# Optimization experiments

Measured on AMD Instinct MI355X. Metric: run time of the kernel, lower is better.

## Reference

```python
import jax, jax.numpy as jnp
import numpy as np

N_NODES = 100000


def setup_inputs() -> dict:
    key = jax.random.key(0)
    k1, k2, k3, k4, k5 = jax.random.split(key, 5)
    dim_in, dim_out = 128, 128
    x = jax.random.normal(k1, (N_NODES, dim_in), dtype=jnp.float32)
    edge_index = jax.random.randint(k2, (2, 1600000), 0, N_NODES, dtype=jnp.int64)
    # PyG SAGEConv params: lin_l (neighbor path, with bias), lin_r (root path, no bias)
    s = 1.0 / np.sqrt(dim_in)
    W_l = jax.random.uniform(k3, (dim_in, dim_out), jnp.float32, -s, s)
    b_l = jax.random.uniform(k4, (dim_out,), jnp.float32, -s, s)
    W_r = jax.random.uniform(k5, (dim_in, dim_out), jnp.float32, -s, s)
    return {"x": x, "edge_index": edge_index, "W_l": W_l, "b_l": b_l, "W_r": W_r}


def reference(x, edge_index, W_l, b_l, W_r):
    src, dst = edge_index[0], edge_index[1]
    # mean aggregation of source features onto target nodes
    gathered = x[src]                                   # [E, d_in]
    summed = jax.ops.segment_sum(gathered, dst, num_segments=N_NODES)
    ones = jnp.ones((edge_index.shape[1],), dtype=x.dtype)
    count = jax.ops.segment_sum(ones, dst, num_segments=N_NODES)
    agg = summed / jnp.maximum(count, 1.0)[:, None]     # [N, d_in]
    # out = lin_l(agg) + lin_r(x)
    return agg @ W_l + b_l + x @ W_r
```

## Files before the change

### kernel.cpp

```cpp
#include <hip/hip_runtime.h>

#define N_NODES 100000
#define DIM 128
#define NE 1600000
#define NTILES (N_NODES / 8)
#define GEMM_BLOCKS 2048
#define CHUNK 512
#define NCHUNK ((N_NODES + CHUNK - 1) / CHUNK)
#define NBKT 1024
#define NBUCKETS ((N_NODES + 127) / 128)
#define NBLK_BIN 200
#define EPB (NE / NBLK_BIN)
#define AGG_CAP 8192

typedef unsigned short u16;
typedef __attribute__((ext_vector_type(8))) short bf16x8;
typedef __attribute__((ext_vector_type(4))) float f32x4;

__device__ __forceinline__ float bf2f(u16 h) {
  return __uint_as_float(((unsigned int)h) << 16);
}
__device__ __forceinline__ u16 f2bf(float f) {
  unsigned int u = __float_as_uint(f);
  unsigned int lsb = (u >> 16) & 1u;
  u += 0x7fffu + lsb;
  return (u16)(u >> 16);
}


__global__ __launch_bounds__(256) void convert_k(const float* __restrict__ x,
                                                 u16* __restrict__ A) {
  int t = blockIdx.x * 256 + threadIdx.x;
  int row = t >> 5;
  int c = (t & 31) * 4;
  float4 v = *(const float4*)(x + (size_t)row * DIM + c);
  ushort4 o;
  o.x = f2bf(v.x); o.y = f2bf(v.y); o.z = f2bf(v.z); o.w = f2bf(v.w);
  *(ushort4*)(A + (size_t)row * 256 + c) = o;
}

__global__ __launch_bounds__(256) void hist1024_k(const int* __restrict__ ei,
                                                  int* __restrict__ gh) {
  __shared__ int h[NBKT];
  for (int i = threadIdx.x; i < NBKT; i += 256) h[i] = 0;
  __syncthreads();
  int e0 = blockIdx.x * EPB;
  for (int i = threadIdx.x; i < EPB; i += 256)
    atomicAdd(&h[ei[NE + e0 + i] >> 7], 1);
  __syncthreads();
  for (int i = threadIdx.x; i < NBKT; i += 256)
    if (h[i]) atomicAdd(&gh[i], h[i]);
}

__global__ __launch_bounds__(1024) void scan1024_k(const int* __restrict__ gh,
                                                   int* __restrict__ base,
                                                   int* __restrict__ cur) {
  __shared__ int s[NBKT];
  int t = threadIdx.x;
  int v = gh[t];
  s[t] = v;
  __syncthreads();
  for (int off = 1; off < NBKT; off <<= 1) {
    int add = (t >= off) ? s[t - off] : 0;
    __syncthreads();
    s[t] += add;
    __syncthreads();
  }
  int excl = s[t] - v;
  base[t] = excl;
  cur[t] = excl;
  if (t == 0) base[NBKT] = NE;
}

__global__ __launch_bounds__(256) void scatter_bin_k(const int* __restrict__ ei,
                                                     int* __restrict__ cur,
                                                     uint2* __restrict__ binned) {
  __shared__ int h[NBKT];
  __shared__ int bbase[NBKT];
  for (int i = threadIdx.x; i < NBKT; i += 256) h[i] = 0;
  __syncthreads();
  int e0 = blockIdx.x * EPB;
  for (int i = threadIdx.x; i < EPB; i += 256)
    atomicAdd(&h[ei[NE + e0 + i] >> 7], 1);
  __syncthreads();
  for (int i = threadIdx.x; i < NBKT; i += 256) {
    int c = h[i];
    bbase[i] = c ? atomicAdd(&cur[i], c) : 0;
    h[i] = 0;
  }
  __syncthreads();
  for (int i = threadIdx.x; i < EPB; i += 256) {
    int src = ei[e0 + i];
    int dst = ei[NE + e0 + i];
    int b = dst >> 7;
    int l = atomicAdd(&h[b], 1);
    binned[bbase[b] + l] = make_uint2((unsigned)src, (unsigned)dst);
  }
}

__global__ __launch_bounds__(256) void aggB_k(const int* __restrict__ base,
                                              const uint2* __restrict__ binned,
                                              u16* __restrict__ A) {
  __shared__ int srcS[AGG_CAP];
  __shared__ int hist[128];
  __shared__ int off[128];
  __shared__ int cur[128];
  const int b = blockIdx.x;
  const int lo = base[b];
  int cnt = base[b + 1] - lo;
  if (cnt > AGG_CAP) cnt = AGG_CAP;

  if (threadIdx.x < 128) hist[threadIdx.x] = 0;
  __syncthreads();
  for (int i = threadIdx.x; i < cnt; i += 256)
    atomicAdd(&hist[binned[lo + i].y & 127], 1);
  __syncthreads();
  if (threadIdx.x < 128) off[threadIdx.x] = hist[threadIdx.x];
  __syncthreads();
  for (int st = 1; st < 128; st <<= 1) {
    int add = 0;
    if (threadIdx.x < 128 && threadIdx.x >= st) add = off[threadIdx.x - st];
    __syncthreads();
    if (threadIdx.x < 128) off[threadIdx.x] += add;
    __syncthreads();
  }
  if (threadIdx.x < 128) cur[threadIdx.x] = off[threadIdx.x] - hist[threadIdx.x];
  __syncthreads();
  for (int i = threadIdx.x; i < cnt; i += 256) {
    uint2 e = binned[lo + i];
    int l = atomicAdd(&cur[e.y & 127], 1);
    srcS[l] = (int)e.x;
  }
  __syncthreads();

  const int wid = threadIdx.x >> 6;
  const int lane = threadIdx.x & 63;
  const int node0 = b * 128;
  for (int ln = wid; ln < 128; ln += 4) {
    int node = node0 + ln;
    if (node >= N_NODES) break;
    int d = hist[ln];
    int e1 = off[ln];
    int j = e1 - d;
    float ax = 0.f, ay = 0.f;
    for (; j + 4 <= e1; j += 4) {
      int s0 = srcS[j], s1 = srcS[j + 1], s2 = srcS[j + 2], s3 = srcS[j + 3];
      unsigned u0 = *(const unsigned*)(A + (size_t)s0 * 256 + lane * 2);
      unsigned u1 = *(const unsigned*)(A + (size_t)s1 * 256 + lane * 2);
      unsigned u2 = *(const unsigned*)(A + (size_t)s2 * 256 + lane * 2);
      unsigned u3 = *(const unsigned*)(A + (size_t)s3 * 256 + lane * 2);
      ax += bf2f((u16)u0) + bf2f((u16)u1) + bf2f((u16)u2) + bf2f((u16)u3);
      ay += bf2f((u16)(u0 >> 16)) + bf2f((u16)(u1 >> 16)) +
            bf2f((u16)(u2 >> 16)) + bf2f((u16)(u3 >> 16));
    }
    for (; j < e1; ++j) {
      unsigned u0 = *(const unsigned*)(A + (size_t)srcS[j] * 256 + lane * 2);
      ax += bf2f((u16)u0);
      ay += bf2f((u16)(u0 >> 16));
    }
    float scale = 1.0f / fmaxf((float)d, 1.0f);
    unsigned p = (unsigned)f2bf(ax * scale) | ((unsigned)f2bf(ay * scale) << 16);
    *(unsigned*)(A + (size_t)node * 256 + 128 + lane * 2) = p;
  }
}

__global__ __launch_bounds__(256) void wt_k(const float* __restrict__ Wl,
                                            const float* __restrict__ Wr,
                                            u16* __restrict__ Wt) {
  int n = blockIdx.x;
  int k = threadIdx.x;
  float v = (k < 128) ? Wr[(size_t)k * DIM + n] : Wl[(size_t)(k - 128) * DIM + n];
  Wt[(size_t)n * 256 + k] = f2bf(v);
}

__global__ __launch_bounds__(256) void gemm_mfma(const u16* __restrict__ A,
                                                 const u16* __restrict__ Wt,
                                                 const float* __restrict__ bias,
                                                 float* __restrict__ out) {
  const int wave = threadIdx.x >> 6;
  const int lane = threadIdx.x & 63;
  const int m = lane & 15;
  const int q = lane >> 4;
  const int n0 = wave * 32;

  bf16x8 Bf[2][8];
#pragma unroll
  for (int t = 0; t < 2; ++t) {
    const u16* bp = Wt + (size_t)(n0 + t * 16 + m) * 256 + q * 8;
#pragma unroll
    for (int s = 0; s < 8; ++s) Bf[t][s] = *(const bf16x8*)(bp + s * 32);
  }
  const float b0 = bias[n0 + m];
  const float b1 = bias[n0 + 16 + m];

  for (int rt = blockIdx.x; rt < N_NODES / 16; rt += gridDim.x) {
    const int row0 = rt * 16;
    const u16* ap = A + (size_t)(row0 + m) * 256 + q * 8;
    bf16x8 Af[8];
#pragma unroll
    for (int s = 0; s < 8; ++s) Af[s] = *(const bf16x8*)(ap + s * 32);
    f32x4 acc0 = {0.f, 0.f, 0.f, 0.f};
    f32x4 acc1 = {0.f, 0.f, 0.f, 0.f};
#pragma unroll
    for (int s = 0; s < 8; ++s) {
      acc0 = __builtin_amdgcn_mfma_f32_16x16x32_bf16(Af[s], Bf[0][s], acc0, 0, 0, 0);
      acc1 = __builtin_amdgcn_mfma_f32_16x16x32_bf16(Af[s], Bf[1][s], acc1, 0, 0, 0);
    }
    float* o = out + (size_t)(row0 + q * 4) * DIM + n0 + m;
#pragma unroll
    for (int r = 0; r < 4; ++r) {
      o[(size_t)r * DIM] = acc0[r] + b0;
      o[(size_t)r * DIM + 16] = acc1[r] + b1;
    }
  }
}

__global__ __launch_bounds__(256) void hist_k(const int* __restrict__ ei,
                                              int* __restrict__ deg) {
  int e = blockIdx.x * 256 + threadIdx.x;
  if (e < NE) atomicAdd(&deg[ei[NE + e]], 1);
}

__global__ __launch_bounds__(512) void scan_sum_k(const int* __restrict__ deg,
                                                  int* __restrict__ partials) {
  __shared__ int s[CHUNK];
  int i = blockIdx.x * CHUNK + threadIdx.x;
  s[threadIdx.x] = (i < N_NODES) ? deg[i] : 0;
  __syncthreads();
  for (int off = 256; off > 0; off >>= 1) {
    if (threadIdx.x < off) s[threadIdx.x] += s[threadIdx.x + off];
    __syncthreads();
  }
  if (threadIdx.x == 0) partials[blockIdx.x] = s[0];
}

__global__ __launch_bounds__(256) void scan_part_k(int* __restrict__ partials) {
  __shared__ int s[256];
  int t = threadIdx.x;
  int v = (t < NCHUNK) ? partials[t] : 0;
  s[t] = v;
  __syncthreads();
  for (int off = 1; off < 256; off <<= 1) {
    int add = (t >= off) ? s[t - off] : 0;
    __syncthreads();
    s[t] += add;
    __syncthreads();
  }
  if (t < NCHUNK) partials[t] = s[t] - v;
}

__global__ __launch_bounds__(512) void scan_out_k(const int* __restrict__ deg,
                                                  const int* __restrict__ partials,
                                                  int* __restrict__ offsets,
                                                  int* __restrict__ cursor) {
  __shared__ int s[CHUNK];
  int t = threadIdx.x;
  int i = blockIdx.x * CHUNK + t;
  int v = (i < N_NODES) ? deg[i] : 0;
  s[t] = v;
  __syncthreads();
  for (int off = 1; off < CHUNK; off <<= 1) {
    int add = (t >= off) ? s[t - off] : 0;
    __syncthreads();
    s[t] += add;
    __syncthreads();
  }
  if (i < N_NODES) {
    int excl = partials[blockIdx.x] + s[t] - v;
    offsets[i] = excl;
    cursor[i] = excl;
  }
  if (i == 0) offsets[N_NODES] = NE;
}

__global__ __launch_bounds__(256) void fill_k(const int* __restrict__ ei,
                                              int* __restrict__ cursor,
                                              int* __restrict__ csr) {
  int e = blockIdx.x * 256 + threadIdx.x;
  if (e < NE) {
    int dst = ei[NE + e];
    int pos = atomicAdd(&cursor[dst], 1);
    csr[pos] = ei[e];
  }
}

__global__ __launch_bounds__(256) void agg_f32_k(const int* __restrict__ offsets,
                                                 const int* __restrict__ csr,
                                                 const float* __restrict__ x,
                                                 float* __restrict__ agg) {
  int node = blockIdx.x * 4 + (threadIdx.x >> 6);
  int lane = threadIdx.x & 63;
  int beg = offsets[node], end = offsets[node + 1];
  float ax = 0.f, ay = 0.f;
  int i = beg;
  for (; i + 4 <= end; i += 4) {
    int s0 = csr[i], s1 = csr[i + 1], s2 = csr[i + 2], s3 = csr[i + 3];
    float2 v0 = *(const float2*)(x + (size_t)s0 * DIM + lane * 2);
    float2 v1 = *(const float2*)(x + (size_t)s1 * DIM + lane * 2);
    float2 v2 = *(const float2*)(x + (size_t)s2 * DIM + lane * 2);
    float2 v3 = *(const float2*)(x + (size_t)s3 * DIM + lane * 2);
    ax += v0.x + v1.x + v2.x + v3.x;
    ay += v0.y + v1.y + v2.y + v3.y;
  }
  for (; i < end; ++i) {
    float2 v0 = *(const float2*)(x + (size_t)csr[i] * DIM + lane * 2);
    ax += v0.x;
    ay += v0.y;
  }
  float scale = 1.0f / fmaxf((float)(end - beg), 1.0f);
  float2 r;
  r.x = ax * scale;
  r.y = ay * scale;
  *(float2*)(agg + (size_t)node * DIM + lane * 2) = r;
}

__global__ __launch_bounds__(256) void gemm_xw(const float* __restrict__ x,
                                               const float* __restrict__ W,
                                               const float* __restrict__ b,
                                               float* __restrict__ out) {
  __shared__ float Ws[DIM * DIM];
  for (int i = threadIdx.x; i < DIM * DIM; i += 256) Ws[i] = W[i];
  __syncthreads();
  const int c = threadIdx.x & 127;
  const int half = threadIdx.x >> 7;
  const float bias = b[c];
  for (int tile = blockIdx.x; tile < NTILES; tile += gridDim.x) {
    const int row0 = tile * 8 + half * 4;
    const float* r = x + (size_t)row0 * DIM;
    float a0 = 0.f, a1 = 0.f, a2 = 0.f, a3 = 0.f;
#pragma unroll 8
    for (int k4 = 0; k4 < 32; ++k4) {
      float4 p0 = *(const float4*)(r + 0 * DIM + k4 * 4);
      float4 p1 = *(const float4*)(r + 1 * DIM + k4 * 4);
      float4 p2 = *(const float4*)(r + 2 * DIM + k4 * 4);
      float4 p3 = *(const float4*)(r + 3 * DIM + k4 * 4);
      const float* wp = &Ws[k4 * 4 * DIM + c];
      float w0 = wp[0 * DIM], w1 = wp[1 * DIM], w2 = wp[2 * DIM], w3 = wp[3 * DIM];
      a0 += p0.x * w0 + p0.y * w1 + p0.z * w2 + p0.w * w3;
      a1 += p1.x * w0 + p1.y * w1 + p1.z * w2 + p1.w * w3;
      a2 += p2.x * w0 + p2.y * w1 + p2.z * w2 + p2.w * w3;
      a3 += p3.x * w0 + p3.y * w1 + p3.z * w2 + p3.w * w3;
    }
    out[(size_t)(row0 + 0) * DIM + c] = a0 + bias;
    out[(size_t)(row0 + 1) * DIM + c] = a1 + bias;
    out[(size_t)(row0 + 2) * DIM + c] = a2 + bias;
    out[(size_t)(row0 + 3) * DIM + c] = a3 + bias;
  }
}

__global__ __launch_bounds__(256) void gemm_aw(const float* __restrict__ agg,
                                               const float* __restrict__ W,
                                               float* __restrict__ out) {
  __shared__ float Ws[DIM * DIM];
  for (int i = threadIdx.x; i < DIM * DIM; i += 256) Ws[i] = W[i];
  __syncthreads();
  const int c = threadIdx.x & 127;
  const int half = threadIdx.x >> 7;
  for (int tile = blockIdx.x; tile < NTILES; tile += gridDim.x) {
    const int row0 = tile * 8 + half * 4;
    const float* r = agg + (size_t)row0 * DIM;
    float a0 = 0.f, a1 = 0.f, a2 = 0.f, a3 = 0.f;
#pragma unroll 8
    for (int k4 = 0; k4 < 32; ++k4) {
      float4 p0 = *(const float4*)(r + 0 * DIM + k4 * 4);
      float4 p1 = *(const float4*)(r + 1 * DIM + k4 * 4);
      float4 p2 = *(const float4*)(r + 2 * DIM + k4 * 4);
      float4 p3 = *(const float4*)(r + 3 * DIM + k4 * 4);
      const float* wp = &Ws[k4 * 4 * DIM + c];
      float w0 = wp[0 * DIM], w1 = wp[1 * DIM], w2 = wp[2 * DIM], w3 = wp[3 * DIM];
      a0 += p0.x * w0 + p0.y * w1 + p0.z * w2 + p0.w * w3;
      a1 += p1.x * w0 + p1.y * w1 + p1.z * w2 + p1.w * w3;
      a2 += p2.x * w0 + p2.y * w1 + p2.z * w2 + p2.w * w3;
      a3 += p3.x * w0 + p3.y * w1 + p3.z * w2 + p3.w * w3;
    }
    out[(size_t)(row0 + 0) * DIM + c] += a0;
    out[(size_t)(row0 + 1) * DIM + c] += a1;
    out[(size_t)(row0 + 2) * DIM + c] += a2;
    out[(size_t)(row0 + 3) * DIM + c] += a3;
  }
}

extern "C" void kernel_launch(void* const* d_in, const int* in_sizes, int n_in,
                              void* d_out, int out_size, void* d_ws, size_t ws_size,
                              hipStream_t stream) {
  const float* x  = (const float*)d_in[0];
  const int*   ei = (const int*)d_in[1];
  const float* Wl = (const float*)d_in[2];
  const float* bl = (const float*)d_in[3];
  const float* Wr = (const float*)d_in[4];
  float* out = (float*)d_out;

  u16* A         = (u16*)d_ws;
  u16* Wt        = A + (size_t)N_NODES * 256;
  uint2* binned  = (uint2*)(Wt + 128 * 256);
  int* bktHist   = (int*)(binned + NE);
  int* bktBase   = bktHist + NBKT;
  int* bktCur    = bktBase + NBKT + 1;
  size_t needed  = (size_t)N_NODES * 512 + 65536 + (size_t)NE * 8 +
                   (NBKT + NBKT + 1 + NBKT) * 4;

  if (ws_size >= needed) {
    hipMemsetAsync(bktHist, 0, NBKT * sizeof(int), stream);
    hipLaunchKernelGGL(convert_k, dim3(12500), dim3(256), 0, stream, x, A);
    hipLaunchKernelGGL(hist1024_k, dim3(NBLK_BIN), dim3(256), 0, stream, ei, bktHist);
    hipLaunchKernelGGL(scan1024_k, dim3(1), dim3(1024), 0, stream,
                       bktHist, bktBase, bktCur);
    hipLaunchKernelGGL(scatter_bin_k, dim3(NBLK_BIN), dim3(256), 0, stream,
                       ei, bktCur, binned);
    hipLaunchKernelGGL(aggB_k, dim3(NBUCKETS), dim3(256), 0, stream,
                       bktBase, binned, A);
    hipLaunchKernelGGL(wt_k, dim3(128), dim3(256), 0, stream, Wl, Wr, Wt);
    hipLaunchKernelGGL(gemm_mfma, dim3(1280), dim3(256), 0, stream,
                       A, Wt, bl, out);
  } else {
    int* deg2      = (int*)d_ws;
    int* offsets2  = deg2 + N_NODES;
    int* partials2 = offsets2 + 100004;
    int* csr2      = partials2 + 256;
    float* agg     = (float*)(csr2 + NE);
    hipMemsetAsync(deg2, 0, (size_t)N_NODES * sizeof(int), stream);
    hipLaunchKernelGGL(hist_k, dim3((NE + 255) / 256), dim3(256), 0, stream, ei, deg2);
    hipLaunchKernelGGL(scan_sum_k, dim3(NCHUNK), dim3(CHUNK), 0, stream, deg2, partials2);
    hipLaunchKernelGGL(scan_part_k, dim3(1), dim3(256), 0, stream, partials2);
    hipLaunchKernelGGL(scan_out_k, dim3(NCHUNK), dim3(CHUNK), 0, stream,
                       deg2, partials2, offsets2, deg2);
    hipLaunchKernelGGL(fill_k, dim3((NE + 255) / 256), dim3(256), 0, stream,
                       ei, deg2, csr2);
    hipLaunchKernelGGL(agg_f32_k, dim3(N_NODES / 4), dim3(256), 0, stream,
                       offsets2, csr2, x, agg);
    hipLaunchKernelGGL(gemm_xw, dim3(GEMM_BLOCKS), dim3(256), 0, stream,
                       x, Wr, bl, out);
    hipLaunchKernelGGL(gemm_aw, dim3(GEMM_BLOCKS), dim3(256), 0, stream,
                       agg, Wl, out);
  }
}
```

Baseline: 291.3 us.

## Pack binned edges into 32-bit records and shrink buckets to 64 nodes

Each binned edge record shrinks from an 8-byte (src,dst) pair to one 32-bit word holding the source index and the destination's low 6 bits. Buckets drop from 128 to 64 nodes, giving 2048 buckets and twice as many aggregation blocks with a smaller shared-memory staging buffer. The scan now has each thread handle two buckets. This halves the scatter write and aggregation read traffic and may raise occupancy, but the per-bucket cap of 2048 edges is tighter and could silently truncate a bucket with high in-degree.

```diff
diff --git a/kernel.cpp b/kernel.cpp
--- a/kernel.cpp
+++ b/kernel.cpp
@@ -7,11 +7,11 @@
 #define GEMM_BLOCKS 2048
 #define CHUNK 512
 #define NCHUNK ((N_NODES + CHUNK - 1) / CHUNK)
-#define NBKT 1024
-#define NBUCKETS ((N_NODES + 127) / 128)
+#define NBKT2 2048
+#define NB64 ((N_NODES + 63) / 64)
 #define NBLK_BIN 200
 #define EPB (NE / NBLK_BIN)
-#define AGG_CAP 8192
+#define BK_CAP 2048
 
 typedef unsigned short u16;
 typedef __attribute__((ext_vector_type(8))) short bf16x8;
@@ -39,51 +39,51 @@
   *(ushort4*)(A + (size_t)row * 256 + c) = o;
 }
 
-__global__ __launch_bounds__(256) void hist1024_k(const int* __restrict__ ei,
+__global__ __launch_bounds__(256) void hist2048_k(const int* __restrict__ ei,
                                                   int* __restrict__ gh) {
-  __shared__ int h[NBKT];
-  for (int i = threadIdx.x; i < NBKT; i += 256) h[i] = 0;
+  __shared__ int h[NBKT2];
+  for (int i = threadIdx.x; i < NBKT2; i += 256) h[i] = 0;
   __syncthreads();
   int e0 = blockIdx.x * EPB;
   for (int i = threadIdx.x; i < EPB; i += 256)
-    atomicAdd(&h[ei[NE + e0 + i] >> 7], 1);
-  __syncthreads();
-  for (int i = threadIdx.x; i < NBKT; i += 256)
+    atomicAdd(&h[ei[NE + e0 + i] >> 6], 1);
+  __syncthreads();
+  for (int i = threadIdx.x; i < NBKT2; i += 256)
     if (h[i]) atomicAdd(&gh[i], h[i]);
 }
 
-__global__ __launch_bounds__(1024) void scan1024_k(const int* __restrict__ gh,
+__global__ __launch_bounds__(1024) void scan2048_k(const int* __restrict__ gh,
                                                    int* __restrict__ base,
                                                    int* __restrict__ cur) {
-  __shared__ int s[NBKT];
+  __shared__ int p[1024];
   int t = threadIdx.x;
-  int v = gh[t];
-  s[t] = v;
-  __syncthreads();
-  for (int off = 1; off < NBKT; off <<= 1) {
-    int add = (t >= off) ? s[t - off] : 0;
-    __syncthreads();
-    s[t] += add;
-    __syncthreads();
-  }
-  int excl = s[t] - v;
-  base[t] = excl;
-  cur[t] = excl;
-  if (t == 0) base[NBKT] = NE;
+  int a = gh[2 * t], b = gh[2 * t + 1];
+  p[t] = a + b;
+  __syncthreads();
+  for (int off = 1; off < 1024; off <<= 1) {
+    int add = (t >= off) ? p[t - off] : 0;
+    __syncthreads();
+    p[t] += add;
+    __syncthreads();
+  }
+  int e0 = p[t] - (a + b);
+  base[2 * t] = e0;       cur[2 * t] = e0;
+  base[2 * t + 1] = e0 + a; cur[2 * t + 1] = e0 + a;
+  if (t == 1023) base[NBKT2] = p[t];
 }
 
 __global__ __launch_bounds__(256) void scatter_bin_k(const int* __restrict__ ei,
                                                      int* __restrict__ cur,
-                                                     uint2* __restrict__ binned) {
-  __shared__ int h[NBKT];
-  __shared__ int bbase[NBKT];
-  for (int i = threadIdx.x; i < NBKT; i += 256) h[i] = 0;
+                                                     int* __restrict__ binned) {
+  __shared__ int h[NBKT2];
+  __shared__ int bbase[NBKT2];
+  for (int i = threadIdx.x; i < NBKT2; i += 256) h[i] = 0;
   __syncthreads();
   int e0 = blockIdx.x * EPB;
   for (int i = threadIdx.x; i < EPB; i += 256)
-    atomicAdd(&h[ei[NE + e0 + i] >> 7], 1);
-  __syncthreads();
-  for (int i = threadIdx.x; i < NBKT; i += 256) {
+    atomicAdd(&h[ei[NE + e0 + i] >> 6], 1);
+  __syncthreads();
+  for (int i = threadIdx.x; i < NBKT2; i += 256) {
     int c = h[i];
     bbase[i] = c ? atomicAdd(&cur[i], c) : 0;
     h[i] = 0;
@@ -92,51 +92,51 @@
   for (int i = threadIdx.x; i < EPB; i += 256) {
     int src = ei[e0 + i];
     int dst = ei[NE + e0 + i];
-    int b = dst >> 7;
+    int b = dst >> 6;
     int l = atomicAdd(&h[b], 1);
-    binned[bbase[b] + l] = make_uint2((unsigned)src, (unsigned)dst);
+    binned[bbase[b] + l] = ((dst & 63) << 17) | src;
   }
 }
 
 __global__ __launch_bounds__(256) void aggB_k(const int* __restrict__ base,
-                                              const uint2* __restrict__ binned,
+                                              const int* __restrict__ binned,
                                               u16* __restrict__ A) {
-  __shared__ int srcS[AGG_CAP];
-  __shared__ int hist[128];
-  __shared__ int off[128];
-  __shared__ int cur[128];
+  __shared__ int srcS[BK_CAP];
+  __shared__ int hist[64];
+  __shared__ int off[64];
+  __shared__ int cur[64];
   const int b = blockIdx.x;
   const int lo = base[b];
   int cnt = base[b + 1] - lo;
-  if (cnt > AGG_CAP) cnt = AGG_CAP;
-
-  if (threadIdx.x < 128) hist[threadIdx.x] = 0;
+  if (cnt > BK_CAP) cnt = BK_CAP;
+
+  if (threadIdx.x < 64) hist[threadIdx.x] = 0;
   __syncthreads();
   for (int i = threadIdx.x; i < cnt; i += 256)
-    atomicAdd(&hist[binned[lo + i].y & 127], 1);
-  __syncthreads();
-  if (threadIdx.x < 128) off[threadIdx.x] = hist[threadIdx.x];
-  __syncthreads();
-  for (int st = 1; st < 128; st <<= 1) {
+    atomicAdd(&hist[binned[lo + i] >> 17], 1);
+  __syncthreads();
+  if (threadIdx.x < 64) off[threadIdx.x] = hist[threadIdx.x];
+  __syncthreads();
+  for (int st = 1; st < 64; st <<= 1) {
     int add = 0;
-    if (threadIdx.x < 128 && threadIdx.x >= st) add = off[threadIdx.x - st];
-    __syncthreads();
-    if (threadIdx.x < 128) off[threadIdx.x] += add;
-    __syncthreads();
-  }
-  if (threadIdx.x < 128) cur[threadIdx.x] = off[threadIdx.x] - hist[threadIdx.x];
+    if (threadIdx.x < 64 && threadIdx.x >= st) add = off[threadIdx.x - st];
+    __syncthreads();
+    if (threadIdx.x < 64) off[threadIdx.x] += add;
+    __syncthreads();
+  }
+  if (threadIdx.x < 64) cur[threadIdx.x] = off[threadIdx.x] - hist[threadIdx.x];
   __syncthreads();
   for (int i = threadIdx.x; i < cnt; i += 256) {
-    uint2 e = binned[lo + i];
-    int l = atomicAdd(&cur[e.y & 127], 1);
-    srcS[l] = (int)e.x;
+    int rec = binned[lo + i];
+    int l = atomicAdd(&cur[rec >> 17], 1);
+    srcS[l] = rec & 0x1FFFF;
   }
   __syncthreads();
 
   const int wid = threadIdx.x >> 6;
   const int lane = threadIdx.x & 63;
-  const int node0 = b * 128;
-  for (int ln = wid; ln < 128; ln += 4) {
+  const int node0 = b * 64;
+  for (int ln = wid; ln < 64; ln += 4) {
     int node = node0 + ln;
     if (node >= N_NODES) break;
     int d = hist[ln];
@@ -390,24 +390,24 @@
   const float* Wr = (const float*)d_in[4];
   float* out = (float*)d_out;
 
-  u16* A         = (u16*)d_ws;
-  u16* Wt        = A + (size_t)N_NODES * 256;
-  uint2* binned  = (uint2*)(Wt + 128 * 256);
-  int* bktHist   = (int*)(binned + NE);
-  int* bktBase   = bktHist + NBKT;
-  int* bktCur    = bktBase + NBKT + 1;
-  size_t needed  = (size_t)N_NODES * 512 + 65536 + (size_t)NE * 8 +
-                   (NBKT + NBKT + 1 + NBKT) * 4;
+  u16* A        = (u16*)d_ws;
+  u16* Wt       = A + (size_t)N_NODES * 256;
+  int* binned   = (int*)(Wt + 128 * 256);
+  int* bktHist  = binned + NE;
+  int* bktBase  = bktHist + NBKT2;
+  int* bktCur   = bktBase + NBKT2 + 1;
+  size_t needed = (size_t)N_NODES * 512 + 65536 + (size_t)NE * 4 +
+                  (NBKT2 + NBKT2 + 1 + NBKT2) * 4;
 
   if (ws_size >= needed) {
-    hipMemsetAsync(bktHist, 0, NBKT * sizeof(int), stream);
+    hipMemsetAsync(bktHist, 0, NBKT2 * sizeof(int), stream);
     hipLaunchKernelGGL(convert_k, dim3(12500), dim3(256), 0, stream, x, A);
-    hipLaunchKernelGGL(hist1024_k, dim3(NBLK_BIN), dim3(256), 0, stream, ei, bktHist);
-    hipLaunchKernelGGL(scan1024_k, dim3(1), dim3(1024), 0, stream,
+    hipLaunchKernelGGL(hist2048_k, dim3(NBLK_BIN), dim3(256), 0, stream, ei, bktHist);
+    hipLaunchKernelGGL(scan2048_k, dim3(1), dim3(1024), 0, stream,
                        bktHist, bktBase, bktCur);
     hipLaunchKernelGGL(scatter_bin_k, dim3(NBLK_BIN), dim3(256), 0, stream,
                        ei, bktCur, binned);
-    hipLaunchKernelGGL(aggB_k, dim3(NBUCKETS), dim3(256), 0, stream,
+    hipLaunchKernelGGL(aggB_k, dim3(NB64), dim3(256), 0, stream,
                        bktBase, binned, A);
     hipLaunchKernelGGL(wt_k, dim3(128), dim3(256), 0, stream, Wl, Wr, Wt);
     hipLaunchKernelGGL(gemm_mfma, dim3(1280), dim3(256), 0, stream,
```

New measurement: 270.8 us. 1.08x faster.
